# Optimization experiments

Measured on AMD Instinct MI355X. Metric: run time of the kernel, lower is better.

## Reference

```python
import jax, jax.numpy as jnp
import numpy as np

B, T, MED, LAB, GLU, D = 1024, 25, 145, 1956, 16, 64
H = D // 2  # 32


def _gat(h, adj, w, a):
    # h: [B, MED, 1] drug-usage counts; in_features=1 so Wh = h * w
    Wh = h * w  # [B, MED, D]
    f1 = Wh @ a[:D]  # [B, MED]
    f2 = Wh @ a[D:]  # [B, MED]
    e = jax.nn.leaky_relu(f1[:, :, None] + f2[:, None, :], 0.2)  # [B, MED, MED]
    e = jnp.where(adj > 0, e, jnp.float32(-9e15))
    attn = jax.nn.softmax(e, axis=-1)
    return jax.nn.elu(attn @ Wh)  # [B, MED, D]


def _mha(q, k, v, wq, wk, wv, wo, nh=4):
    Bq, Lq, Dm = q.shape
    dh = Dm // nh
    qh = (q @ wq).reshape(Bq, Lq, nh, dh)
    kh = (k @ wk).reshape(Bq, k.shape[1], nh, dh)
    vh = (v @ wv).reshape(Bq, v.shape[1], nh, dh)
    s = jnp.einsum('bqhd,bkhd->bhqk', qh, kh) / np.float32(np.sqrt(dh))
    a = jax.nn.softmax(s, axis=-1)
    o = jnp.einsum('bhqk,bkhd->bqhd', a, vh).reshape(Bq, Lq, Dm)
    return o @ wo


def _gated(x, g):
    # Attn_encoder: per-position gated emphasis, preserves sequence shape
    return x * jax.nn.sigmoid(x @ g)[..., None]


def setup_inputs():
    key = jax.random.key(0)
    ks = jax.random.split(key, 40)
    n = lambda i, shape, s=0.05: (jax.random.normal(ks[i], shape, dtype=jnp.float32) * s)
    inp = {
        'lab': jax.random.normal(ks[0], (B, LAB), dtype=jnp.float32),
        'glu': jax.random.normal(ks[1], (B, T, GLU), dtype=jnp.float32),
        'time_feat': jax.random.uniform(ks[2], (B, T, GLU), dtype=jnp.float32),
        'med': jax.random.uniform(ks[3], (B, T, MED), dtype=jnp.float32),
        'ehr_adj': (jax.random.uniform(ks[4], (MED, MED)) > 0.9).astype(jnp.float32),
        'ddi_adj': (jax.random.uniform(ks[5], (MED, MED)) > 0.9).astype(jnp.float32),
        'time_adj': (jax.random.uniform(ks[6], (MED, MED)) > 0.9).astype(jnp.float32),
        'sll_w1': n(7, (LAB, D)), 'sll_b1': n(8, (D,)),
        'sll_w2': n(9, (D, H)), 'sll_b2': n(10, (H,)),
        'glu_w': n(11, (2 * GLU, H)), 'glu_b': n(12, (H,)), 'glu_gate': n(13, (H,)),
        'med_w': n(14, (MED, D)), 'med_b': n(15, (D,)), 'med_gate': n(16, (D,)),
        'gat_ehr_w': n(17, (D,)), 'gat_ehr_a': n(18, (2 * D,)),
        'gat_time_w': n(19, (D,)), 'gat_time_a': n(20, (2 * D,)),
        'gat_ddi_w': n(21, (D,)), 'gat_ddi_a': n(22, (2 * D,)),
        'ga_wq': n(23, (D, D)), 'ga_wk': n(24, (D, D)), 'ga_wv': n(25, (D, D)), 'ga_wo': n(26, (D, D)),
        'm1_wq': n(27, (D, D)), 'm1_wk': n(28, (D, D)), 'm1_wv': n(29, (D, D)), 'm1_wo': n(30, (D, D)),
        'm2_wq': n(31, (D, D)), 'm2_wk': n(32, (D, D)), 'm2_wv': n(33, (D, D)), 'm2_wo': n(34, (D, D)),
        'out_w1': n(35, (MED * D, MED * D // 8), 0.01), 'out_b1': n(36, (MED * D // 8,)),
        'out_w2': n(37, (MED * D // 8, MED)), 'out_b2': n(38, (MED,)),
    }
    return inp


def reference(lab, glu, time_feat, med, ehr_adj, ddi_adj, time_adj,
              sll_w1, sll_b1, sll_w2, sll_b2,
              glu_w, glu_b, glu_gate, med_w, med_b, med_gate,
              gat_ehr_w, gat_ehr_a, gat_time_w, gat_time_a, gat_ddi_w, gat_ddi_a,
              ga_wq, ga_wk, ga_wv, ga_wo,
              m1_wq, m1_wk, m1_wv, m1_wo,
              m2_wq, m2_wk, m2_wv, m2_wo,
              out_w1, out_b1, out_w2, out_b2):
    relu = jax.nn.relu
    medb = (med > 0.9).astype(med.dtype)  # multi-hot medication history
    # static_ll, repeated over visits
    static = relu(relu(lab @ sll_w1 + sll_b1) @ sll_w2 + sll_b2)  # [B, H]
    static_seq = jnp.broadcast_to(static[:, None, :], (B, T, H))
    # per-patient drug usage counts over past visits
    h = jnp.sum(medb[:, :-1], axis=1)[..., None]  # [B, MED, 1]
    g_ehr = _gat(h, ehr_adj, gat_ehr_w, gat_ehr_a)
    g_time = _gat(h, time_adj, gat_time_w, gat_time_a)
    g_ddi = _gat(h, ddi_adj, gat_ddi_w, gat_ddi_a)
    all_graph = jnp.concatenate([g_ehr, g_time, g_ddi], axis=1)  # [B, 3*MED, D]
    dm = _mha(all_graph, all_graph, all_graph, ga_wq, ga_wk, ga_wv, ga_wo)
    drug_mem = dm.reshape(B, 3, MED, D).mean(axis=1)  # [B, MED, D]
    # medication / glucose encoders
    med_rep = _gated(medb[:, :-1] @ med_w + med_b, med_gate)  # [B, T-1, D]
    glu_in = jnp.concatenate([glu, time_feat], axis=-1)  # [B, T, 2*GLU]
    glu_rep = _gated(jnp.tanh(glu_in @ glu_w + glu_b), glu_gate)  # [B, T, H]
    patient = jnp.concatenate([glu_rep, static_seq], axis=-1)  # [B, T, D]
    # m1: query = med history, keys/values = patient visits
    E_en = _mha(med_rep, patient, patient, m1_wq, m1_wk, m1_wv, m1_wo)  # [B, T-1, D]
    e0 = E_en[:, :1]  # [B, 1, D]
    # m2: query = drug memory, keys/values = encoded state
    E_de = _mha(drug_mem, e0, e0, m2_wq, m2_wk, m2_wv, m2_wo)  # [B, MED, D]
    final = E_de.reshape(B, MED * D)
    hid = relu(relu(final) @ out_w1 + out_b1)
    return hid @ out_w2 + out_b2  # [B, MED]
```

## Files before the change

### kernel.cpp

```cpp
#include <hip/hip_runtime.h>
#include <math.h>

#define B_   1024
#define T_   25
#define MED_ 145
#define LAB_ 1956
#define GLU_ 16
#define D_   64
#define H_   32
#define HID_ 1160
#define KC_  978

__global__ __launch_bounds__(512) void k_static_a(
    const float* __restrict__ lab, const float* __restrict__ w1,
    float* __restrict__ part) {
  const int rg = blockIdx.x;
  const int kc = blockIdx.y;
  const int b0 = rg * 4;
  const int k0 = kc * KC_;
  const int tid = threadIdx.x;
  __shared__ float2 lab_s2[4][KC_ / 2];
  for (int e = tid; e < 4 * (KC_ / 2); e += 512) {
    int r = e / (KC_ / 2), i = e - r * (KC_ / 2);
    lab_s2[r][i] = ((const float2*)(lab + (size_t)(b0 + r) * LAB_ + k0))[i];
  }
  __syncthreads();
  const float* lab_f = (const float*)lab_s2;
  const int col = tid & 63;
  const int slice = tid >> 6;
  float a0 = 0.f, a1 = 0.f, a2 = 0.f, a3 = 0.f;
  #pragma unroll 4
  for (int k = slice; k < KC_; k += 8) {
    float w = w1[(size_t)(k0 + k) * D_ + col];
    a0 = fmaf(lab_f[k], w, a0);
    a1 = fmaf(lab_f[KC_ + k], w, a1);
    a2 = fmaf(lab_f[2 * KC_ + k], w, a2);
    a3 = fmaf(lab_f[3 * KC_ + k], w, a3);
  }
  __syncthreads();
  __shared__ float red[4][8][64];
  red[0][slice][col] = a0;
  red[1][slice][col] = a1;
  red[2][slice][col] = a2;
  red[3][slice][col] = a3;
  __syncthreads();
  if (tid < 256) {
    int r = tid >> 6, d = tid & 63;
    float v = 0.f;
    #pragma unroll
    for (int s2 = 0; s2 < 8; ++s2) v += red[r][s2][d];
    part[(size_t)kc * B_ * D_ + (size_t)(b0 + r) * D_ + d] = v;
  }
}

__global__ __launch_bounds__(256) void k_static_b(
    const float* __restrict__ part, const float* __restrict__ b1,
    const float* __restrict__ w2, const float* __restrict__ b2,
    float* __restrict__ st) {
  const int b0 = blockIdx.x * 4;
  const int tid = threadIdx.x;
  __shared__ float t1[4][64];
  {
    int r = tid >> 6, d = tid & 63;
    size_t o = (size_t)(b0 + r) * D_ + d;
    float v = part[o] + part[(size_t)B_ * D_ + o] + b1[d];
    t1[r][d] = fmaxf(v, 0.f);
  }
  __syncthreads();
  if (tid < 128) {
    int r = tid >> 5, j = tid & 31;
    float s = b2[j];
    #pragma unroll 8
    for (int d = 0; d < D_; ++d) s = fmaf(t1[r][d], w2[d * H_ + j], s);
    st[(size_t)(b0 + r) * H_ + j] = fmaxf(s, 0.f);
  }
}

__global__ __launch_bounds__(256) void k_w1c(const float* __restrict__ w1,
                                             float* __restrict__ w1c) {
  const int idx = blockIdx.x * 256 + threadIdx.x;
  const int mq = blockIdx.y;
  const int m0 = (mq * MED_) >> 2, m1 = ((mq + 1) * MED_) >> 2;
  const float* p = w1 + idx + (size_t)m0 * D_ * HID_;
  float s = 0.f;
  #pragma unroll 8
  for (int m = m0; m < m1; ++m) {
    s += *p;
    p += (size_t)D_ * HID_;
  }
  atomicAdd(&w1c[idx], s);
}

__global__ __launch_bounds__(256) void k_perb(
    const float* __restrict__ glu, const float* __restrict__ tf,
    const float* __restrict__ med, const float* __restrict__ st,
    const float* __restrict__ glu_w, const float* __restrict__ glu_b,
    const float* __restrict__ glu_gate, const float* __restrict__ med_w,
    const float* __restrict__ med_b, const float* __restrict__ med_gate,
    const float* __restrict__ wq, const float* __restrict__ wk,
    const float* __restrict__ wv, const float* __restrict__ wo,
    const float* __restrict__ m2wv, const float* __restrict__ m2wo,
    float* __restrict__ rr) {
  const int b = blockIdx.x;
  const int tid = threadIdx.x;
  const int d = tid & 63;
  const int s4 = tid >> 6;
  __shared__ float xin_s[T_][2 * GLU_];
  __shared__ float y_s[T_][H_];
  __shared__ float gate_s[T_];
  __shared__ float medrow_s[MED_];
  __shared__ float pat_s[28][D_];
  __shared__ float q0_s[D_];
  __shared__ float kh_s[T_][D_];
  __shared__ float vh_s[T_][D_];
  __shared__ float sc_s[4][T_];
  __shared__ float at_s[4][T_];
  __shared__ float o_s[D_];
  __shared__ float vec_s[D_];
  __shared__ float red4[4][D_];

  for (int e = tid; e < T_ * GLU_; e += 256) {
    int t = e >> 4, i = e & 15;
    xin_s[t][i] = glu[((size_t)b * T_ + t) * GLU_ + i];
    xin_s[t][GLU_ + i] = tf[((size_t)b * T_ + t) * GLU_ + i];
  }
  if (tid < MED_) medrow_s[tid] = med[(size_t)b * T_ * MED_ + tid];
  __syncthreads();

  for (int e = tid; e < T_ * H_; e += 256) {
    int t = e >> 5, j = e & 31;
    float s = glu_b[j];
    #pragma unroll 8
    for (int i = 0; i < 2 * GLU_; ++i) s = fmaf(xin_s[t][i], glu_w[i * H_ + j], s);
    y_s[t][j] = tanhf(s);
  }
  __syncthreads();

  if (tid < T_) {
    float s = 0.f;
    #pragma unroll 8
    for (int j = 0; j < H_; ++j) s = fmaf(y_s[tid][j], glu_gate[j], s);
    gate_s[tid] = 1.f / (1.f + __expf(-s));
  }
  if (tid >= 64 && tid < 128) {
    int dd = tid - 64;
    float x = med_b[dd];
    for (int m = 0; m < MED_; ++m)
      if (medrow_s[m] > 0.9f) x += med_w[m * D_ + dd];
    float v = x * med_gate[dd];
    #pragma unroll
    for (int off = 32; off > 0; off >>= 1) v += __shfl_xor(v, off);
    q0_s[dd] = x * (1.f / (1.f + __expf(-v)));
  }
  __syncthreads();

  for (int e = tid; e < 28 * H_; e += 256) {
    int t = e >> 5, j = e & 31;
    if (t < T_) {
      pat_s[t][j] = y_s[t][j] * gate_s[t];
      pat_s[t][H_ + j] = st[(size_t)b * H_ + j];
    } else {
      pat_s[t][j] = 0.f;
      pat_s[t][H_ + j] = 0.f;
    }
  }
  __syncthreads();

  {
    float aK[7] = {0.f, 0.f, 0.f, 0.f, 0.f, 0.f, 0.f};
    float aV[7] = {0.f, 0.f, 0.f, 0.f, 0.f, 0.f, 0.f};
    #pragma unroll 4
    for (int j = 0; j < D_; ++j) {
      float wkj = wk[j * D_ + d];
      float wvj = wv[j * D_ + d];
      #pragma unroll
      for (int i = 0; i < 7; ++i) {
        float p = pat_s[s4 + 4 * i][j];
        aK[i] = fmaf(p, wkj, aK[i]);
        aV[i] = fmaf(p, wvj, aV[i]);
      }
    }
    #pragma unroll
    for (int i = 0; i < 7; ++i) {
      int t = s4 + 4 * i;
      if (t < T_) { kh_s[t][d] = aK[i]; vh_s[t][d] = aV[i]; }
    }
  }
  {
    float qp = 0.f;
    #pragma unroll
    for (int i = 0; i < 16; ++i) {
      int j = s4 * 16 + i;
      qp = fmaf(q0_s[j], wq[j * D_ + d], qp);
    }
    red4[s4][d] = qp;
  }
  __syncthreads();
  if (tid < D_) vec_s[tid] = red4[0][tid] + red4[1][tid] + red4[2][tid] + red4[3][tid];
  __syncthreads();

  if (tid < 4 * T_) {
    int h = tid / T_, t = tid - h * T_;
    float s = 0.f;
    #pragma unroll
    for (int i = 0; i < 16; ++i) s = fmaf(vec_s[h * 16 + i], kh_s[t][h * 16 + i], s);
    sc_s[h][t] = s * 0.25f;
  }
  __syncthreads();
  if (tid < 4) {
    float m = -1e30f;
    for (int t = 0; t < T_; ++t) m = fmaxf(m, sc_s[tid][t]);
    float sum = 0.f;
    for (int t = 0; t < T_; ++t) {
      float e = __expf(sc_s[tid][t] - m);
      at_s[tid][t] = e;
      sum += e;
    }
    float inv = 1.f / sum;
    for (int t = 0; t < T_; ++t) at_s[tid][t] *= inv;
  }
  __syncthreads();
  if (tid < D_) {
    int h = tid >> 4;
    float s = 0.f;
    #pragma unroll
    for (int t = 0; t < T_; ++t) s = fmaf(at_s[h][t], vh_s[t][tid], s);
    o_s[tid] = s;
  }
  __syncthreads();
  {
    float p = 0.f;
    #pragma unroll
    for (int i = 0; i < 16; ++i) {
      int j = s4 * 16 + i;
      p = fmaf(o_s[j], wo[j * D_ + d], p);
    }
    red4[s4][d] = p;
  }
  __syncthreads();
  if (tid < D_) vec_s[tid] = red4[0][tid] + red4[1][tid] + red4[2][tid] + red4[3][tid];
  __syncthreads();
  {
    float p = 0.f;
    #pragma unroll
    for (int i = 0; i < 16; ++i) {
      int j = s4 * 16 + i;
      p = fmaf(vec_s[j], m2wv[j * D_ + d], p);
    }
    red4[s4][d] = p;
  }
  __syncthreads();
  if (tid < D_) o_s[tid] = red4[0][tid] + red4[1][tid] + red4[2][tid] + red4[3][tid];
  __syncthreads();
  {
    float p = 0.f;
    #pragma unroll
    for (int i = 0; i < 16; ++i) {
      int j = s4 * 16 + i;
      p = fmaf(o_s[j], m2wo[j * D_ + d], p);
    }
    red4[s4][d] = p;
  }
  __syncthreads();
  if (tid < D_) {
    float v = red4[0][tid] + red4[1][tid] + red4[2][tid] + red4[3][tid];
    rr[(size_t)b * D_ + tid] = fmaxf(v, 0.f);
  }
}

__global__ __launch_bounds__(640) void k_final(
    const float* __restrict__ rr, const float* __restrict__ w1c,
    const float* __restrict__ b1, const float* __restrict__ w2,
    const float* __restrict__ b2, float* __restrict__ out) {
  __shared__ float rr_s[2][D_];
  __shared__ float hid_s[2][HID_];
  __shared__ float p2_s[2][2][152];
  const int tid = threadIdx.x;
  const int b0 = blockIdx.x * 2;
  if (tid < 128) rr_s[tid >> 6][tid & 63] = rr[(size_t)b0 * D_ + tid];
  __syncthreads();
  for (int e = tid; e < 2 * HID_; e += 640) {
    int r = e / HID_, j = e - r * HID_;
    float s = b1[j];
    #pragma unroll 8
    for (int dd = 0; dd < D_; ++dd) s = fmaf(rr_s[r][dd], w1c[(size_t)dd * HID_ + j], s);
    hid_s[r][j] = fmaxf(s, 0.f);
  }
  __syncthreads();
  if (tid < 580) {
    int h = tid / 290, rem = tid - h * 290;
    int rh = rem / MED_, n = rem - rh * MED_;
    const float* hp = hid_s[rh] + h * 580;
    const float* wp = w2 + (size_t)h * 580 * MED_ + n;
    float s = 0.f;
    #pragma unroll 8
    for (int j = 0; j < 580; ++j) s = fmaf(hp[j], wp[(size_t)j * MED_], s);
    p2_s[h][rh][n] = s;
  }
  __syncthreads();
  if (tid < 2 * MED_) {
    int rh = tid / MED_, n = tid - rh * MED_;
    out[(size_t)(b0 + rh) * MED_ + n] = p2_s[0][rh][n] + p2_s[1][rh][n] + b2[n];
  }
}

extern "C" void kernel_launch(void* const* d_in, const int* in_sizes, int n_in,
                              void* d_out, int out_size, void* d_ws, size_t ws_size,
                              hipStream_t stream) {
  (void)in_sizes; (void)n_in; (void)out_size; (void)ws_size;
  const float* lab      = (const float*)d_in[0];
  const float* glu      = (const float*)d_in[1];
  const float* tf       = (const float*)d_in[2];
  const float* med      = (const float*)d_in[3];
  const float* sll_w1   = (const float*)d_in[7];
  const float* sll_b1   = (const float*)d_in[8];
  const float* sll_w2   = (const float*)d_in[9];
  const float* sll_b2   = (const float*)d_in[10];
  const float* glu_w    = (const float*)d_in[11];
  const float* glu_b    = (const float*)d_in[12];
  const float* glu_gate = (const float*)d_in[13];
  const float* med_w    = (const float*)d_in[14];
  const float* med_b    = (const float*)d_in[15];
  const float* med_gate = (const float*)d_in[16];
  const float* m1_wq    = (const float*)d_in[27];
  const float* m1_wk    = (const float*)d_in[28];
  const float* m1_wv    = (const float*)d_in[29];
  const float* m1_wo    = (const float*)d_in[30];
  const float* m2_wv    = (const float*)d_in[33];
  const float* m2_wo    = (const float*)d_in[34];
  const float* out_w1   = (const float*)d_in[35];
  const float* out_b1   = (const float*)d_in[36];
  const float* out_w2   = (const float*)d_in[37];
  const float* out_b2   = (const float*)d_in[38];
  float* out = (float*)d_out;

  float* ws   = (float*)d_ws;
  float* st   = ws;
  float* rr   = st + B_ * H_;
  float* w1c  = rr + B_ * D_;
  float* part = w1c + D_ * HID_;

  hipLaunchKernelGGL(k_static_a, dim3(B_ / 4, 2), dim3(512), 0, stream,
                     lab, sll_w1, part);
  hipLaunchKernelGGL(k_static_b, dim3(B_ / 4), dim3(256), 0, stream,
                     part, sll_b1, sll_w2, sll_b2, st);
  hipMemsetAsync(w1c, 0, (size_t)D_ * HID_ * sizeof(float), stream);
  hipLaunchKernelGGL(k_w1c, dim3((D_ * HID_) / 256, 4), dim3(256), 0, stream,
                     out_w1, w1c);
  hipLaunchKernelGGL(k_perb, dim3(B_), dim3(256), 0, stream,
                     glu, tf, med, st, glu_w, glu_b, glu_gate,
                     med_w, med_b, med_gate,
                     m1_wq, m1_wk, m1_wv, m1_wo, m2_wv, m2_wo, rr);
  hipLaunchKernelGGL(k_final, dim3(B_ / 2), dim3(640), 0, stream,
                     rr, w1c, out_b1, out_w2, out_b2, out);
}
```

Measured before the change: 276.0 us.

## Tile final MLP over batch rows and hidden splits with atomic accumulation

The final MLP kernel now handles 16 batch rows per block and splits the 1160-wide hidden dimension into four slices across blockIdx.y. Each weight load from w1c and w2 is reused across 8 or 4 rows, and partial outputs are combined with atomicAdd into an output zeroed by a new memset. The static-lab GEMV doubles its rows per block to 8 for more weight reuse. The per-batch kernel spreads the medication-sum and gate dot products over more threads. The cost is atomics, an extra memset, and more registers per thread.

```diff
diff --git a/kernel.cpp b/kernel.cpp
--- a/kernel.cpp
+++ b/kernel.cpp
@@ -14,13 +14,12 @@
 __global__ __launch_bounds__(512) void k_static_a(
     const float* __restrict__ lab, const float* __restrict__ w1,
     float* __restrict__ part) {
-  const int rg = blockIdx.x;
+  const int b0 = blockIdx.x * 8;
   const int kc = blockIdx.y;
-  const int b0 = rg * 4;
   const int k0 = kc * KC_;
   const int tid = threadIdx.x;
-  __shared__ float2 lab_s2[4][KC_ / 2];
-  for (int e = tid; e < 4 * (KC_ / 2); e += 512) {
+  __shared__ float2 lab_s2[8][KC_ / 2];
+  for (int e = tid; e < 8 * (KC_ / 2); e += 512) {
     int r = e / (KC_ / 2), i = e - r * (KC_ / 2);
     lab_s2[r][i] = ((const float2*)(lab + (size_t)(b0 + r) * LAB_ + k0))[i];
   }
@@ -28,23 +27,19 @@
   const float* lab_f = (const float*)lab_s2;
   const int col = tid & 63;
   const int slice = tid >> 6;
-  float a0 = 0.f, a1 = 0.f, a2 = 0.f, a3 = 0.f;
-  #pragma unroll 4
+  float acc[8] = {0.f, 0.f, 0.f, 0.f, 0.f, 0.f, 0.f, 0.f};
+  #pragma unroll 2
   for (int k = slice; k < KC_; k += 8) {
     float w = w1[(size_t)(k0 + k) * D_ + col];
-    a0 = fmaf(lab_f[k], w, a0);
-    a1 = fmaf(lab_f[KC_ + k], w, a1);
-    a2 = fmaf(lab_f[2 * KC_ + k], w, a2);
-    a3 = fmaf(lab_f[3 * KC_ + k], w, a3);
-  }
-  __syncthreads();
-  __shared__ float red[4][8][64];
-  red[0][slice][col] = a0;
-  red[1][slice][col] = a1;
-  red[2][slice][col] = a2;
-  red[3][slice][col] = a3;
-  __syncthreads();
-  if (tid < 256) {
+    #pragma unroll
+    for (int r = 0; r < 8; ++r) acc[r] = fmaf(lab_f[r * KC_ + k], w, acc[r]);
+  }
+  __syncthreads();
+  __shared__ float red[8][8][64];
+  #pragma unroll
+  for (int r = 0; r < 8; ++r) red[r][slice][col] = acc[r];
+  __syncthreads();
+  {
     int r = tid >> 6, d = tid & 63;
     float v = 0.f;
     #pragma unroll
@@ -136,24 +131,34 @@
   }
   __syncthreads();
 
-  if (tid < T_) {
+  if (tid < 8 * T_) {
+    int t = tid >> 3, sl = tid & 7;
     float s = 0.f;
-    #pragma unroll 8
-    for (int j = 0; j < H_; ++j) s = fmaf(y_s[tid][j], glu_gate[j], s);
-    gate_s[tid] = 1.f / (1.f + __expf(-s));
-  }
-  if (tid >= 64 && tid < 128) {
-    int dd = tid - 64;
-    float x = med_b[dd];
-    for (int m = 0; m < MED_; ++m)
-      if (medrow_s[m] > 0.9f) x += med_w[m * D_ + dd];
-    float v = x * med_gate[dd];
+    #pragma unroll
+    for (int i = 0; i < 4; ++i) {
+      int j = sl * 4 + i;
+      s = fmaf(y_s[t][j], glu_gate[j], s);
+    }
+    s += __shfl_xor(s, 1);
+    s += __shfl_xor(s, 2);
+    s += __shfl_xor(s, 4);
+    if (sl == 0) gate_s[t] = 1.f / (1.f + __expf(-s));
+  }
+  {
+    float x = 0.f;
+    for (int m = s4; m < MED_; m += 4)
+      if (medrow_s[m] > 0.9f) x += med_w[m * D_ + d];
+    red4[s4][d] = x;
+  }
+  __syncthreads();
+
+  if (tid < D_) {
+    float x = med_b[tid] + red4[0][tid] + red4[1][tid] + red4[2][tid] + red4[3][tid];
+    float v = x * med_gate[tid];
     #pragma unroll
     for (int off = 32; off > 0; off >>= 1) v += __shfl_xor(v, off);
-    q0_s[dd] = x * (1.f / (1.f + __expf(-v)));
-  }
-  __syncthreads();
-
+    q0_s[tid] = x * (1.f / (1.f + __expf(-v)));
+  }
   for (int e = tid; e < 28 * H_; e += 256) {
     int t = e >> 5, j = e & 31;
     if (t < T_) {
@@ -272,35 +277,69 @@
     const float* __restrict__ rr, const float* __restrict__ w1c,
     const float* __restrict__ b1, const float* __restrict__ w2,
     const float* __restrict__ b2, float* __restrict__ out) {
-  __shared__ float rr_s[2][D_];
-  __shared__ float hid_s[2][HID_];
-  __shared__ float p2_s[2][2][152];
   const int tid = threadIdx.x;
-  const int b0 = blockIdx.x * 2;
-  if (tid < 128) rr_s[tid >> 6][tid & 63] = rr[(size_t)b0 * D_ + tid];
-  __syncthreads();
-  for (int e = tid; e < 2 * HID_; e += 640) {
-    int r = e / HID_, j = e - r * HID_;
-    float s = b1[j];
-    #pragma unroll 8
-    for (int dd = 0; dd < D_; ++dd) s = fmaf(rr_s[r][dd], w1c[(size_t)dd * HID_ + j], s);
-    hid_s[r][j] = fmaxf(s, 0.f);
-  }
+  const int b0 = blockIdx.x * 16;
+  const int jq = blockIdx.y;
+  const int j0 = jq * 290;
+  __shared__ float rr_s[16][D_];
+  __shared__ float hid_s[16][292];
+  for (int e = tid; e < 16 * D_; e += 640)
+    ((float*)rr_s)[e] = rr[(size_t)b0 * D_ + e];
   __syncthreads();
   if (tid < 580) {
-    int h = tid / 290, rem = tid - h * 290;
-    int rh = rem / MED_, n = rem - rh * MED_;
-    const float* hp = hid_s[rh] + h * 580;
-    const float* wp = w2 + (size_t)h * 580 * MED_ + n;
-    float s = 0.f;
-    #pragma unroll 8
-    for (int j = 0; j < 580; ++j) s = fmaf(hp[j], wp[(size_t)j * MED_], s);
-    p2_s[h][rh][n] = s;
-  }
-  __syncthreads();
-  if (tid < 2 * MED_) {
-    int rh = tid / MED_, n = tid - rh * MED_;
-    out[(size_t)(b0 + rh) * MED_ + n] = p2_s[0][rh][n] + p2_s[1][rh][n] + b2[n];
+    int jj = tid % 290, rh = tid / 290;
+    const float* wp = w1c + (size_t)(j0 + jj);
+    float bb = b1[j0 + jj];
+    float acc[8] = {0.f, 0.f, 0.f, 0.f, 0.f, 0.f, 0.f, 0.f};
+    #pragma unroll 4
+    for (int d4 = 0; d4 < 16; ++d4) {
+      float w0 = wp[(size_t)(4 * d4 + 0) * HID_];
+      float w1v = wp[(size_t)(4 * d4 + 1) * HID_];
+      float w2v = wp[(size_t)(4 * d4 + 2) * HID_];
+      float w3v = wp[(size_t)(4 * d4 + 3) * HID_];
+      #pragma unroll
+      for (int r8 = 0; r8 < 8; ++r8) {
+        float4 rv = *(const float4*)&rr_s[rh * 8 + r8][4 * d4];
+        acc[r8] += rv.x * w0 + rv.y * w1v + rv.z * w2v + rv.w * w3v;
+      }
+    }
+    #pragma unroll
+    for (int r8 = 0; r8 < 8; ++r8)
+      hid_s[rh * 8 + r8][jj] = fmaxf(acc[r8] + bb, 0.f);
+  }
+  __syncthreads();
+  if (tid < 580) {
+    int n = tid % MED_, rg = tid / MED_;
+    const float* w2p = w2 + (size_t)j0 * MED_ + n;
+    float s0 = 0.f, s1 = 0.f, s2 = 0.f, s3 = 0.f;
+    #pragma unroll 4
+    for (int jv = 0; jv < 72; ++jv) {
+      float wa = w2p[(size_t)(4 * jv + 0) * MED_];
+      float wb = w2p[(size_t)(4 * jv + 1) * MED_];
+      float wc = w2p[(size_t)(4 * jv + 2) * MED_];
+      float wd = w2p[(size_t)(4 * jv + 3) * MED_];
+      float4 h0 = *(const float4*)&hid_s[rg * 4 + 0][4 * jv];
+      float4 h1 = *(const float4*)&hid_s[rg * 4 + 1][4 * jv];
+      float4 h2 = *(const float4*)&hid_s[rg * 4 + 2][4 * jv];
+      float4 h3 = *(const float4*)&hid_s[rg * 4 + 3][4 * jv];
+      s0 += h0.x * wa + h0.y * wb + h0.z * wc + h0.w * wd;
+      s1 += h1.x * wa + h1.y * wb + h1.z * wc + h1.w * wd;
+      s2 += h2.x * wa + h2.y * wb + h2.z * wc + h2.w * wd;
+      s3 += h3.x * wa + h3.y * wb + h3.z * wc + h3.w * wd;
+    }
+    {
+      float wa = w2p[(size_t)288 * MED_];
+      float wb = w2p[(size_t)289 * MED_];
+      s0 += hid_s[rg * 4 + 0][288] * wa + hid_s[rg * 4 + 0][289] * wb;
+      s1 += hid_s[rg * 4 + 1][288] * wa + hid_s[rg * 4 + 1][289] * wb;
+      s2 += hid_s[rg * 4 + 2][288] * wa + hid_s[rg * 4 + 2][289] * wb;
+      s3 += hid_s[rg * 4 + 3][288] * wa + hid_s[rg * 4 + 3][289] * wb;
+    }
+    float bias = (jq == 0) ? b2[n] : 0.f;
+    atomicAdd(&out[(size_t)(b0 + rg * 4 + 0) * MED_ + n], s0 + bias);
+    atomicAdd(&out[(size_t)(b0 + rg * 4 + 1) * MED_ + n], s1 + bias);
+    atomicAdd(&out[(size_t)(b0 + rg * 4 + 2) * MED_ + n], s2 + bias);
+    atomicAdd(&out[(size_t)(b0 + rg * 4 + 3) * MED_ + n], s3 + bias);
   }
 }
 
@@ -340,17 +379,18 @@
   float* w1c  = rr + B_ * D_;
   float* part = w1c + D_ * HID_;
 
-  hipLaunchKernelGGL(k_static_a, dim3(B_ / 4, 2), dim3(512), 0, stream,
+  hipLaunchKernelGGL(k_static_a, dim3(B_ / 8, 2), dim3(512), 0, stream,
                      lab, sll_w1, part);
   hipLaunchKernelGGL(k_static_b, dim3(B_ / 4), dim3(256), 0, stream,
                      part, sll_b1, sll_w2, sll_b2, st);
   hipMemsetAsync(w1c, 0, (size_t)D_ * HID_ * sizeof(float), stream);
+  hipMemsetAsync(out, 0, (size_t)B_ * MED_ * sizeof(float), stream);
   hipLaunchKernelGGL(k_w1c, dim3((D_ * HID_) / 256, 4), dim3(256), 0, stream,
                      out_w1, w1c);
   hipLaunchKernelGGL(k_perb, dim3(B_), dim3(256), 0, stream,
                      glu, tf, med, st, glu_w, glu_b, glu_gate,
                      med_w, med_b, med_gate,
                      m1_wq, m1_wk, m1_wv, m1_wo, m2_wv, m2_wo, rr);
-  hipLaunchKernelGGL(k_final, dim3(B_ / 2), dim3(640), 0, stream,
+  hipLaunchKernelGGL(k_final, dim3(B_ / 16, 4), dim3(640), 0, stream,
                      rr, w1c, out_b1, out_w2, out_b2, out);
 }
```

Result: faster. 244.7 us (-11.3%).
